# Optimization experiments

Hardware: AMD Instinct MI355X
Metric: run time of the kernel (lower is better)

## Reference

```python
import jax, jax.numpy as jnp
import numpy as np

M, N, D, B, LAYERS = 512, 512, 1024, 4096, 16


def setup_inputs() -> dict:
    key = jax.random.key(0)
    ks = jax.random.split(key, 4)
    x = jax.random.normal(ks[0], (M, B), dtype=jnp.float32)
    A = jax.random.normal(ks[1], (M, D), dtype=jnp.float32) / np.float32(np.sqrt(M))
    # fc[k].weight = A.t() + 0.001*randn  -> shape [d, m]
    W = A.T[None] + 0.001 * jax.random.normal(ks[2], (LAYERS, D, M), dtype=jnp.float32)
    Z0 = (1.0 / D) * jax.random.uniform(ks[3], (D, B), dtype=jnp.float32)
    E0 = jnp.zeros((M, B), dtype=jnp.float32)
    L0 = jnp.zeros((M, B), dtype=jnp.float32)
    ones = jnp.ones((LAYERS,), dtype=jnp.float32)
    return {
        'x': x, 'A': A, 'W': W, 'Z0': Z0, 'E0': E0, 'L0': L0,
        'beta1': ones, 'beta2': ones, 'beta3': ones, 'ss2': ones,
        'active_para': 0.2 * ones, 'active_para1': 0.8 * ones,
    }


def _soft(v, t):
    # self_active: relu(v - t) - relu(-v - t)  (soft threshold)
    return jax.nn.relu(v - t) - jax.nn.relu(-v - t)


def reference(x, A, W, Z0, E0, L0, beta1, beta2, beta3, ss2, active_para, active_para1):
    K = W.shape[0]
    # k = 0 (learned branch)
    T0 = A @ Z0 + E0 - x                      # [m, B]
    Var0 = L0 + beta1[0] * T0
    Z1 = _soft(Z0 - W[0] @ Var0, active_para[0])  # [d, B]

    def step(carry, params):
        Zp, Ep, Lp = carry
        b1, b2, b3, s2, ap, ap1, Wk = params
        AZ = A @ Zp                            # [m, B]
        VVar = Lp + b2 * (AZ + Ep - x)
        En = _soft(Ep - s2 * VVar, ap1)
        Tn = AZ + En - x
        Ln = Lp + b3 * Tn
        Varn = Ln + b1 * Tn
        Zn = _soft(Zp - Wk @ Varn, ap)
        return (Zn, En, Ln), (Zn, En, Ln)

    params = (beta1[1:], beta2[:K - 1], beta3[:K - 1], ss2[:K - 1],
              active_para[1:], active_para1[:K - 1], W[1:])
    _, (Zs, Es, Ls) = jax.lax.scan(step, (Z1, E0, L0), params)
    Z_all = jnp.concatenate([Z1[None], Zs], axis=0)   # [K, d, B]
    E_all = jnp.concatenate([E0[None], Es], axis=0)   # [K, m, B]
    L_all = jnp.concatenate([L0[None], Ls], axis=0)   # [K, m, B]
    return Z_all, E_all, L_all
```

## Files before the change

kernel.cpp:

```cpp
#include <hip/hip_runtime.h>
#include <cstddef>

#define MDIM 512
#define DDIM 1024
#define BDIM 4096
#define NLAYERS 16

constexpr int BK = 16;

__device__ __forceinline__ float softf(float v, float t) {
  return copysignf(fmaxf(fabsf(v) - t, 0.0f), v);
}

template <int MODE, int K>
__global__ __launch_bounds__(256) void gemm_bc(
    const float* __restrict__ P, const float* __restrict__ Bm,
    const float* __restrict__ xg, const float* __restrict__ Ep,
    const float* __restrict__ Lp, const float* __restrict__ Zp,
    const float* __restrict__ beta1, const float* __restrict__ beta2,
    const float* __restrict__ beta3, const float* __restrict__ ss2,
    const float* __restrict__ apar, const float* __restrict__ apar1, int k,
    float* __restrict__ O0, float* __restrict__ O1, float* __restrict__ O2) {
  __shared__ __align__(16) float As[2][BK][32];
  __shared__ __align__(16) float Bs[2][BK][128];

  const int tid = threadIdx.x;
  const int lane = tid & 63;
  const int w = __builtin_amdgcn_readfirstlane((int)(tid >> 6));
  const int m0 = blockIdx.x * 32, n0 = blockIdx.y * 128;
  const int r0 = m0 + w * 8;
  const int c0 = n0 + lane * 2;

  float acc[8][2];
#pragma unroll
  for (int r = 0; r < 8; ++r) {
    acc[r][0] = 0.0f;
    acc[r][1] = 0.0f;
  }

  const int ar = tid >> 3, akc = (tid & 7) * 2;
  const float* gA = P + (size_t)(m0 + ar) * K + akc;
  const int br = tid >> 4, bc = (tid & 15) * 8;
  const float* gB = Bm + (size_t)br * BDIM + n0 + bc;

  float2 rA;
  float4 rB0, rB1;
  auto gload = [&](int k0) {
    rA = *reinterpret_cast<const float2*>(gA + (size_t)k0);
    rB0 = *reinterpret_cast<const float4*>(gB + (size_t)k0 * BDIM);
    rB1 = *reinterpret_cast<const float4*>(gB + (size_t)k0 * BDIM + 4);
  };
  auto stagewr = [&](int bb) {
    As[bb][akc][ar] = rA.x;
    As[bb][akc + 1][ar] = rA.y;
    *reinterpret_cast<float4*>(&Bs[bb][br][bc]) = rB0;
    *reinterpret_cast<float4*>(&Bs[bb][br][bc + 4]) = rB1;
  };
  auto comp = [&](int bb) {
#pragma unroll
    for (int kk = 0; kk < BK; ++kk) {
      const float4 a0 = *reinterpret_cast<const float4*>(&As[bb][kk][w * 8]);
      const float4 a1 =
          *reinterpret_cast<const float4*>(&As[bb][kk][w * 8 + 4]);
      const float a[8] = {a0.x, a0.y, a0.z, a0.w, a1.x, a1.y, a1.z, a1.w};
      const float2 b2 = *reinterpret_cast<const float2*>(&Bs[bb][kk][lane * 2]);
#pragma unroll
      for (int r = 0; r < 8; ++r) {
        acc[r][0] = fmaf(a[r], b2.x, acc[r][0]);
        acc[r][1] = fmaf(a[r], b2.y, acc[r][1]);
      }
    }
  };

  constexpr int NS = K / BK;
  gload(0);
  stagewr(0);
  __syncthreads();
  int bb = 0;
#pragma unroll 1
  for (int t = 1; t < NS; ++t) {
    gload(t * BK);
    comp(bb);
    stagewr(bb ^ 1);
    __syncthreads();
    bb ^= 1;
  }
  comp(bb);

  const float b1v = (MODE == 2) ? 0.f : beta1[k];
  float b2v = 0.f, b3v = 0.f, s2v = 0.f, a1v = 0.f, ap = 0.f;
  if (MODE == 1) {
    b2v = beta2[k - 1];
    b3v = beta3[k - 1];
    s2v = ss2[k - 1];
    a1v = apar1[k - 1];
  }
  if (MODE == 2) ap = apar[k];

#pragma unroll
  for (int r = 0; r < 8; ++r) {
    const size_t off = (size_t)(r0 + r) * BDIM + c0;
    if (MODE == 2) {
      const float2 z2 = *reinterpret_cast<const float2*>(&Zp[off]);
      float2 o;
      o.x = softf(z2.x - acc[r][0], ap);
      o.y = softf(z2.y - acc[r][1], ap);
      *reinterpret_cast<float2*>(&O0[off]) = o;
    } else {
      const float2 e2 = *reinterpret_cast<const float2*>(&Ep[off]);
      const float2 l2 = *reinterpret_cast<const float2*>(&Lp[off]);
      const float2 x2 = *reinterpret_cast<const float2*>(&xg[off]);
      const float ev[2] = {e2.x, e2.y};
      const float lv[2] = {l2.x, l2.y};
      const float xv[2] = {x2.x, x2.y};
      float vo[2], eo[2], lo_[2];
#pragma unroll
      for (int j = 0; j < 2; ++j) {
        const float az = acc[r][j];
        if (MODE == 0) {
          const float t0 = az + ev[j] - xv[j];
          vo[j] = fmaf(b1v, t0, lv[j]);
          eo[j] = ev[j];
          lo_[j] = lv[j];
        } else {
          const float vv = fmaf(b2v, az + ev[j] - xv[j], lv[j]);
          const float en = softf(ev[j] - s2v * vv, a1v);
          const float tn_ = az + en - xv[j];
          const float ln = fmaf(b3v, tn_, lv[j]);
          eo[j] = en;
          lo_[j] = ln;
          vo[j] = fmaf(b1v, tn_, ln);
        }
      }
      float2 t2;
      t2.x = vo[0];
      t2.y = vo[1];
      *reinterpret_cast<float2*>(&O0[off]) = t2;
      t2.x = eo[0];
      t2.y = eo[1];
      *reinterpret_cast<float2*>(&O1[off]) = t2;
      t2.x = lo_[0];
      t2.y = lo_[1];
      *reinterpret_cast<float2*>(&O2[off]) = t2;
    }
  }
}

extern "C" void kernel_launch(void* const* d_in, const int* in_sizes, int n_in,
                              void* d_out, int out_size, void* d_ws,
                              size_t ws_size, hipStream_t stream) {
  (void)in_sizes;
  (void)n_in;
  (void)out_size;
  (void)ws_size;
  const float* x = (const float*)d_in[0];
  const float* A = (const float*)d_in[1];
  const float* W = (const float*)d_in[2];
  const float* Z0 = (const float*)d_in[3];
  const float* E0 = (const float*)d_in[4];
  const float* L0 = (const float*)d_in[5];
  const float* beta1 = (const float*)d_in[6];
  const float* beta2 = (const float*)d_in[7];
  const float* beta3 = (const float*)d_in[8];
  const float* ss2 = (const float*)d_in[9];
  const float* apar = (const float*)d_in[10];
  const float* apar1 = (const float*)d_in[11];

  constexpr size_t DB = (size_t)DDIM * BDIM;
  constexpr size_t MB = (size_t)MDIM * BDIM;
  float* Zall = (float*)d_out;
  float* Eall = Zall + (size_t)NLAYERS * DB;
  float* Lall = Eall + (size_t)NLAYERS * MB;
  float* Var = (float*)d_ws;

  const dim3 blk(256);
  const dim3 gA(MDIM / 32, BDIM / 128);
  const dim3 gB(DDIM / 32, BDIM / 128);

  gemm_bc<0, DDIM><<<gA, blk, 0, stream>>>(
      A, Z0, x, E0, L0, nullptr, beta1, beta2, beta3, ss2, apar, apar1, 0, Var,
      Eall, Lall);
  gemm_bc<2, MDIM><<<gB, blk, 0, stream>>>(
      W, Var, nullptr, nullptr, nullptr, Z0, beta1, beta2, beta3, ss2, apar,
      apar1, 0, Zall, nullptr, nullptr);
  for (int k = 1; k < NLAYERS; ++k) {
    const float* Zp = Zall + (size_t)(k - 1) * DB;
    gemm_bc<1, DDIM><<<gA, blk, 0, stream>>>(
        A, Zp, x, Eall + (size_t)(k - 1) * MB, Lall + (size_t)(k - 1) * MB,
        nullptr, beta1, beta2, beta3, ss2, apar, apar1, k, Var,
        Eall + (size_t)k * MB, Lall + (size_t)k * MB);
    gemm_bc<2, MDIM><<<gB, blk, 0, stream>>>(
        W + (size_t)k * DDIM * MDIM, Var, nullptr, nullptr, nullptr, Zp, beta1,
        beta2, beta3, ss2, apar, apar1, k, Zall + (size_t)k * DB, nullptr,
        nullptr);
  }
}
```

Baseline: 2.445 ms.

## Shrink GEMM tile rows, add XCD-aware block remapping and occupancy hints

Halves the M-tile from 32 to 16 rows, so each thread now computes a 4x2 output block instead of 8x2 and the grid doubles. Block ids are remapped round-robin across the 8 XCDs so neighbouring tiles share an L2. Launch bounds now request a minimum number of waves per SIMD, and the B shared tile is padded to 132 columns. The intent is more blocks and higher occupancy to hide latency, at the cost of less register reuse per loaded B element and more total global traffic for B.

```diff
diff --git a/kernel.cpp b/kernel.cpp
--- a/kernel.cpp
+++ b/kernel.cpp
@@ -12,8 +12,8 @@
   return copysignf(fmaxf(fabsf(v) - t, 0.0f), v);
 }
 
-template <int MODE, int K>
-__global__ __launch_bounds__(256) void gemm_bc(
+template <int MODE, int K, int LOG2GX, int MINW>
+__global__ __launch_bounds__(256, MINW) void gemm_ho(
     const float* __restrict__ P, const float* __restrict__ Bm,
     const float* __restrict__ xg, const float* __restrict__ Ep,
     const float* __restrict__ Lp, const float* __restrict__ Zp,
@@ -21,51 +21,56 @@
     const float* __restrict__ beta3, const float* __restrict__ ss2,
     const float* __restrict__ apar, const float* __restrict__ apar1, int k,
     float* __restrict__ O0, float* __restrict__ O1, float* __restrict__ O2) {
-  __shared__ __align__(16) float As[2][BK][32];
-  __shared__ __align__(16) float Bs[2][BK][128];
+  __shared__ __align__(16) float As[2][BK][16];
+  __shared__ __align__(16) float Bs[2][BK][132];
 
   const int tid = threadIdx.x;
   const int lane = tid & 63;
   const int w = __builtin_amdgcn_readfirstlane((int)(tid >> 6));
-  const int m0 = blockIdx.x * 32, n0 = blockIdx.y * 128;
-  const int r0 = m0 + w * 8;
+
+  const int nwg = gridDim.x * gridDim.y;
+  const int bid = blockIdx.x + gridDim.x * blockIdx.y;
+  const int cpx = nwg >> 3;
+  const int lgc = (bid & 7) * cpx + (bid >> 3);
+  const int bx = lgc & ((1 << LOG2GX) - 1);
+  const int by = lgc >> LOG2GX;
+
+  const int m0 = bx * 16, n0 = by * 128;
+  const int r0 = m0 + w * 4;
   const int c0 = n0 + lane * 2;
 
-  float acc[8][2];
-#pragma unroll
-  for (int r = 0; r < 8; ++r) {
+  float acc[4][2];
+#pragma unroll
+  for (int r = 0; r < 4; ++r) {
     acc[r][0] = 0.0f;
     acc[r][1] = 0.0f;
   }
 
-  const int ar = tid >> 3, akc = (tid & 7) * 2;
-  const float* gA = P + (size_t)(m0 + ar) * K + akc;
-  const int br = tid >> 4, bc = (tid & 15) * 8;
-  const float* gB = Bm + (size_t)br * BDIM + n0 + bc;
-
-  float2 rA;
+  const int arow = tid >> 4, ak = tid & 15;
+  const float* gA = P + (size_t)(m0 + arow) * K + ak;
+  const int brow = tid >> 4, bcol = (tid & 15) * 8;
+  const float* gB = Bm + (size_t)brow * BDIM + n0 + bcol;
+
+  float rA;
   float4 rB0, rB1;
   auto gload = [&](int k0) {
-    rA = *reinterpret_cast<const float2*>(gA + (size_t)k0);
+    rA = gA[(size_t)k0];
     rB0 = *reinterpret_cast<const float4*>(gB + (size_t)k0 * BDIM);
     rB1 = *reinterpret_cast<const float4*>(gB + (size_t)k0 * BDIM + 4);
   };
   auto stagewr = [&](int bb) {
-    As[bb][akc][ar] = rA.x;
-    As[bb][akc + 1][ar] = rA.y;
-    *reinterpret_cast<float4*>(&Bs[bb][br][bc]) = rB0;
-    *reinterpret_cast<float4*>(&Bs[bb][br][bc + 4]) = rB1;
+    As[bb][ak][arow] = rA;
+    *reinterpret_cast<float4*>(&Bs[bb][brow][bcol]) = rB0;
+    *reinterpret_cast<float4*>(&Bs[bb][brow][bcol + 4]) = rB1;
   };
   auto comp = [&](int bb) {
 #pragma unroll
     for (int kk = 0; kk < BK; ++kk) {
-      const float4 a0 = *reinterpret_cast<const float4*>(&As[bb][kk][w * 8]);
-      const float4 a1 =
-          *reinterpret_cast<const float4*>(&As[bb][kk][w * 8 + 4]);
-      const float a[8] = {a0.x, a0.y, a0.z, a0.w, a1.x, a1.y, a1.z, a1.w};
+      const float4 a4 = *reinterpret_cast<const float4*>(&As[bb][kk][w * 4]);
+      const float a[4] = {a4.x, a4.y, a4.z, a4.w};
       const float2 b2 = *reinterpret_cast<const float2*>(&Bs[bb][kk][lane * 2]);
 #pragma unroll
-      for (int r = 0; r < 8; ++r) {
+      for (int r = 0; r < 4; ++r) {
         acc[r][0] = fmaf(a[r], b2.x, acc[r][0]);
         acc[r][1] = fmaf(a[r], b2.y, acc[r][1]);
       }
@@ -98,7 +103,7 @@
   if (MODE == 2) ap = apar[k];
 
 #pragma unroll
-  for (int r = 0; r < 8; ++r) {
+  for (int r = 0; r < 4; ++r) {
     const size_t off = (size_t)(r0 + r) * BDIM + c0;
     if (MODE == 2) {
       const float2 z2 = *reinterpret_cast<const float2*>(&Zp[off]);
@@ -174,22 +179,22 @@
   float* Var = (float*)d_ws;
 
   const dim3 blk(256);
-  const dim3 gA(MDIM / 32, BDIM / 128);
-  const dim3 gB(DDIM / 32, BDIM / 128);
-
-  gemm_bc<0, DDIM><<<gA, blk, 0, stream>>>(
+  const dim3 gA(MDIM / 16, BDIM / 128);
+  const dim3 gB(DDIM / 16, BDIM / 128);
+
+  gemm_ho<0, DDIM, 5, 4><<<gA, blk, 0, stream>>>(
       A, Z0, x, E0, L0, nullptr, beta1, beta2, beta3, ss2, apar, apar1, 0, Var,
       Eall, Lall);
-  gemm_bc<2, MDIM><<<gB, blk, 0, stream>>>(
+  gemm_ho<2, MDIM, 6, 8><<<gB, blk, 0, stream>>>(
       W, Var, nullptr, nullptr, nullptr, Z0, beta1, beta2, beta3, ss2, apar,
       apar1, 0, Zall, nullptr, nullptr);
   for (int k = 1; k < NLAYERS; ++k) {
     const float* Zp = Zall + (size_t)(k - 1) * DB;
-    gemm_bc<1, DDIM><<<gA, blk, 0, stream>>>(
+    gemm_ho<1, DDIM, 5, 4><<<gA, blk, 0, stream>>>(
         A, Zp, x, Eall + (size_t)(k - 1) * MB, Lall + (size_t)(k - 1) * MB,
         nullptr, beta1, beta2, beta3, ss2, apar, apar1, k, Var,
         Eall + (size_t)k * MB, Lall + (size_t)k * MB);
-    gemm_bc<2, MDIM><<<gB, blk, 0, stream>>>(
+    gemm_ho<2, MDIM, 6, 8><<<gB, blk, 0, stream>>>(
         W + (size_t)k * DDIM * MDIM, Var, nullptr, nullptr, nullptr, Zp, beta1,
         beta2, beta3, ss2, apar, apar1, k, Zall + (size_t)k * DB, nullptr,
         nullptr);
```

Result: slower. 2.779 ms (+13.7%).

## Replace LDS-tiled GEMM with register-only packed-FMA GEMM using larger tiles

Applied to the files above, without the earlier changes.

Removes shared-memory staging and barriers from the GEMM. Each wave now loads its 16 rows of the left matrix directly from global memory; these addresses are wave-uniform, so the loads act as broadcasts. Each lane loads its own two columns of the right operand and accumulates with packed 2-wide FMAs (v_pk_fma_f32), with register double-buffering of k-chunks of two. The block tile grows to 64 rows and the launch grids shrink to match, trading LDS reuse and coalesced staging for many small global loads that lean on the cache, plus higher register pressure.

```diff
diff --git a/kernel.cpp b/kernel.cpp
--- a/kernel.cpp
+++ b/kernel.cpp
@@ -6,14 +6,14 @@
 #define BDIM 4096
 #define NLAYERS 16
 
-constexpr int BK = 16;
+typedef float f32x2 __attribute__((ext_vector_type(2)));
 
 __device__ __forceinline__ float softf(float v, float t) {
   return copysignf(fmaxf(fabsf(v) - t, 0.0f), v);
 }
 
 template <int MODE, int K>
-__global__ __launch_bounds__(256) void gemm_bc(
+__global__ __launch_bounds__(256, 2) void gemm_pk(
     const float* __restrict__ P, const float* __restrict__ Bm,
     const float* __restrict__ xg, const float* __restrict__ Ep,
     const float* __restrict__ Lp, const float* __restrict__ Zp,
@@ -21,71 +21,55 @@
     const float* __restrict__ beta3, const float* __restrict__ ss2,
     const float* __restrict__ apar, const float* __restrict__ apar1, int k,
     float* __restrict__ O0, float* __restrict__ O1, float* __restrict__ O2) {
-  __shared__ __align__(16) float As[2][BK][32];
-  __shared__ __align__(16) float Bs[2][BK][128];
-
   const int tid = threadIdx.x;
   const int lane = tid & 63;
   const int w = __builtin_amdgcn_readfirstlane((int)(tid >> 6));
-  const int m0 = blockIdx.x * 32, n0 = blockIdx.y * 128;
-  const int r0 = m0 + w * 8;
-  const int c0 = n0 + lane * 2;
+  const int m0 = blockIdx.x * 64 + w * 16;
+  const int c0 = blockIdx.y * 128 + lane * 2;
 
-  float acc[8][2];
+  const float* pA = P + (size_t)m0 * K;
+  const float* pB = Bm + c0;
+
+  f32x2 acc[16];
 #pragma unroll
-  for (int r = 0; r < 8; ++r) {
-    acc[r][0] = 0.0f;
-    acc[r][1] = 0.0f;
-  }
+  for (int r = 0; r < 16; ++r) acc[r] = (f32x2)(0.0f);
 
-  const int ar = tid >> 3, akc = (tid & 7) * 2;
-  const float* gA = P + (size_t)(m0 + ar) * K + akc;
-  const int br = tid >> 4, bc = (tid & 15) * 8;
-  const float* gB = Bm + (size_t)br * BDIM + n0 + bc;
+  f32x2 A0[16], A1[16], B0[2], B1[2];
 
-  float2 rA;
-  float4 rB0, rB1;
-  auto gload = [&](int k0) {
-    rA = *reinterpret_cast<const float2*>(gA + (size_t)k0);
-    rB0 = *reinterpret_cast<const float4*>(gB + (size_t)k0 * BDIM);
-    rB1 = *reinterpret_cast<const float4*>(gB + (size_t)k0 * BDIM + 4);
+  auto loadA = [&](f32x2(&Ab)[16], int k0) {
+#pragma unroll
+    for (int r = 0; r < 16; ++r)
+      Ab[r] = *reinterpret_cast<const f32x2*>(pA + (size_t)r * K + k0);
   };
-  auto stagewr = [&](int bb) {
-    As[bb][akc][ar] = rA.x;
-    As[bb][akc + 1][ar] = rA.y;
-    *reinterpret_cast<float4*>(&Bs[bb][br][bc]) = rB0;
-    *reinterpret_cast<float4*>(&Bs[bb][br][bc + 4]) = rB1;
+  auto loadB = [&](f32x2(&Bb)[2], int k0) {
+#pragma unroll
+    for (int j = 0; j < 2; ++j)
+      Bb[j] = *reinterpret_cast<const f32x2*>(pB + (size_t)(k0 + j) * BDIM);
   };
-  auto comp = [&](int bb) {
+  auto comp = [&](const f32x2(&Ab)[16], const f32x2(&Bb)[2]) {
 #pragma unroll
-    for (int kk = 0; kk < BK; ++kk) {
-      const float4 a0 = *reinterpret_cast<const float4*>(&As[bb][kk][w * 8]);
-      const float4 a1 =
-          *reinterpret_cast<const float4*>(&As[bb][kk][w * 8 + 4]);
-      const float a[8] = {a0.x, a0.y, a0.z, a0.w, a1.x, a1.y, a1.z, a1.w};
-      const float2 b2 = *reinterpret_cast<const float2*>(&Bs[bb][kk][lane * 2]);
+    for (int j = 0; j < 2; ++j)
 #pragma unroll
-      for (int r = 0; r < 8; ++r) {
-        acc[r][0] = fmaf(a[r], b2.x, acc[r][0]);
-        acc[r][1] = fmaf(a[r], b2.y, acc[r][1]);
+      for (int r = 0; r < 16; ++r) {
+        const f32x2 av = {Ab[r][j], Ab[r][j]};
+        acc[r] = __builtin_elementwise_fma(av, Bb[j], acc[r]);
       }
-    }
   };
 
-  constexpr int NS = K / BK;
-  gload(0);
-  stagewr(0);
-  __syncthreads();
-  int bb = 0;
+  constexpr int NCH = K / 2;
+  loadA(A0, 0);
+  loadB(B0, 0);
 #pragma unroll 1
-  for (int t = 1; t < NS; ++t) {
-    gload(t * BK);
-    comp(bb);
-    stagewr(bb ^ 1);
-    __syncthreads();
-    bb ^= 1;
+  for (int t = 0; t + 2 <= NCH; t += 2) {
+    loadA(A1, (t + 1) * 2);
+    loadB(B1, (t + 1) * 2);
+    comp(A0, B0);
+    if (t + 2 < NCH) {
+      loadA(A0, (t + 2) * 2);
+      loadB(B0, (t + 2) * 2);
+    }
+    comp(A1, B1);
   }
-  comp(bb);
 
   const float b1v = (MODE == 2) ? 0.f : beta1[k];
   float b2v = 0.f, b3v = 0.f, s2v = 0.f, a1v = 0.f, ap = 0.f;
@@ -98,8 +82,8 @@
   if (MODE == 2) ap = apar[k];
 
 #pragma unroll
-  for (int r = 0; r < 8; ++r) {
-    const size_t off = (size_t)(r0 + r) * BDIM + c0;
+  for (int r = 0; r < 16; ++r) {
+    const size_t off = (size_t)(m0 + r) * BDIM + c0;
     if (MODE == 2) {
       const float2 z2 = *reinterpret_cast<const float2*>(&Zp[off]);
       float2 o;
@@ -174,22 +158,22 @@
   float* Var = (float*)d_ws;
 
   const dim3 blk(256);
-  const dim3 gA(MDIM / 32, BDIM / 128);
-  const dim3 gB(DDIM / 32, BDIM / 128);
+  const dim3 gA(MDIM / 64, BDIM / 128);
+  const dim3 gB(DDIM / 64, BDIM / 128);
 
-  gemm_bc<0, DDIM><<<gA, blk, 0, stream>>>(
+  gemm_pk<0, DDIM><<<gA, blk, 0, stream>>>(
       A, Z0, x, E0, L0, nullptr, beta1, beta2, beta3, ss2, apar, apar1, 0, Var,
       Eall, Lall);
-  gemm_bc<2, MDIM><<<gB, blk, 0, stream>>>(
+  gemm_pk<2, MDIM><<<gB, blk, 0, stream>>>(
       W, Var, nullptr, nullptr, nullptr, Z0, beta1, beta2, beta3, ss2, apar,
       apar1, 0, Zall, nullptr, nullptr);
   for (int k = 1; k < NLAYERS; ++k) {
     const float* Zp = Zall + (size_t)(k - 1) * DB;
-    gemm_bc<1, DDIM><<<gA, blk, 0, stream>>>(
+    gemm_pk<1, DDIM><<<gA, blk, 0, stream>>>(
         A, Zp, x, Eall + (size_t)(k - 1) * MB, Lall + (size_t)(k - 1) * MB,
         nullptr, beta1, beta2, beta3, ss2, apar, apar1, k, Var,
         Eall + (size_t)k * MB, Lall + (size_t)k * MB);
-    gemm_bc<2, MDIM><<<gB, blk, 0, stream>>>(
+    gemm_pk<2, MDIM><<<gB, blk, 0, stream>>>(
         W + (size_t)k * DDIM * MDIM, Var, nullptr, nullptr, nullptr, Zp, beta1,
         beta2, beta3, ss2, apar, apar1, k, Zall + (size_t)k * DB, nullptr,
         nullptr);
```

Result: slower. 6.038 ms (+147.0%).

## Enlarge register tiles per thread in fused GEMM kernels

Applied to the files above, without the earlier changes.

Restructures the GEMM kernel so each thread computes an 8x(2*TNW) register tile instead of 8x2. The block M-tile grows to 64 rows for the A@Z GEMM and 128 rows for the W@Var GEMM. This raises the FMA-to-LDS-load ratio and cuts redundant global traffic on the B operand, which is re-read by fewer blocks. In exchange it uses more registers, which may lower occupancy, and the epilogue stores become strided scalar accesses split into two column groups.

```diff
diff --git a/kernel.cpp b/kernel.cpp
--- a/kernel.cpp
+++ b/kernel.cpp
@@ -12,8 +12,8 @@
   return copysignf(fmaxf(fabsf(v) - t, 0.0f), v);
 }
 
-template <int MODE, int K>
-__global__ __launch_bounds__(256) void gemm_bc(
+template <int MODE, int K, int TNW>
+__global__ __launch_bounds__(256) void gemm_rt(
     const float* __restrict__ P, const float* __restrict__ Bm,
     const float* __restrict__ xg, const float* __restrict__ Ep,
     const float* __restrict__ Lp, const float* __restrict__ Zp,
@@ -21,54 +21,77 @@
     const float* __restrict__ beta3, const float* __restrict__ ss2,
     const float* __restrict__ apar, const float* __restrict__ apar1, int k,
     float* __restrict__ O0, float* __restrict__ O1, float* __restrict__ O2) {
-  __shared__ __align__(16) float As[2][BK][32];
+  constexpr int BM = 32 * TNW;
+  constexpr int CT = 64 / TNW;
+  constexpr int APT = BM / 64;
+  __shared__ __align__(16) float As[2][BK][BM];
   __shared__ __align__(16) float Bs[2][BK][128];
 
   const int tid = threadIdx.x;
-  const int lane = tid & 63;
-  const int w = __builtin_amdgcn_readfirstlane((int)(tid >> 6));
-  const int m0 = blockIdx.x * 32, n0 = blockIdx.y * 128;
-  const int r0 = m0 + w * 8;
-  const int c0 = n0 + lane * 2;
-
-  float acc[8][2];
-#pragma unroll
-  for (int r = 0; r < 8; ++r) {
-    acc[r][0] = 0.0f;
-    acc[r][1] = 0.0f;
-  }
-
-  const int ar = tid >> 3, akc = (tid & 7) * 2;
+  const int tn = tid & (CT - 1);
+  const int tm = tid / CT;
+  const int m0 = blockIdx.x * BM, n0 = blockIdx.y * 128;
+
+  float acc[8][2][TNW];
+#pragma unroll
+  for (int r = 0; r < 8; ++r)
+#pragma unroll
+    for (int g = 0; g < 2; ++g)
+#pragma unroll
+      for (int j = 0; j < TNW; ++j) acc[r][g][j] = 0.0f;
+
+  const int ar = (APT == 1) ? (tid >> 2) : (tid >> 1);
+  const int akc = (APT == 1) ? ((tid & 3) * 4) : ((tid & 1) * 8);
   const float* gA = P + (size_t)(m0 + ar) * K + akc;
   const int br = tid >> 4, bc = (tid & 15) * 8;
   const float* gB = Bm + (size_t)br * BDIM + n0 + bc;
 
-  float2 rA;
-  float4 rB0, rB1;
+  float4 rA0, rA1, rB0, rB1;
   auto gload = [&](int k0) {
-    rA = *reinterpret_cast<const float2*>(gA + (size_t)k0);
+    rA0 = *reinterpret_cast<const float4*>(gA + (size_t)k0);
+    if (APT == 2) rA1 = *reinterpret_cast<const float4*>(gA + (size_t)k0 + 4);
     rB0 = *reinterpret_cast<const float4*>(gB + (size_t)k0 * BDIM);
     rB1 = *reinterpret_cast<const float4*>(gB + (size_t)k0 * BDIM + 4);
   };
   auto stagewr = [&](int bb) {
-    As[bb][akc][ar] = rA.x;
-    As[bb][akc + 1][ar] = rA.y;
+    As[bb][akc + 0][ar] = rA0.x;
+    As[bb][akc + 1][ar] = rA0.y;
+    As[bb][akc + 2][ar] = rA0.z;
+    As[bb][akc + 3][ar] = rA0.w;
+    if (APT == 2) {
+      As[bb][akc + 4][ar] = rA1.x;
+      As[bb][akc + 5][ar] = rA1.y;
+      As[bb][akc + 6][ar] = rA1.z;
+      As[bb][akc + 7][ar] = rA1.w;
+    }
     *reinterpret_cast<float4*>(&Bs[bb][br][bc]) = rB0;
     *reinterpret_cast<float4*>(&Bs[bb][br][bc + 4]) = rB1;
   };
   auto comp = [&](int bb) {
 #pragma unroll
     for (int kk = 0; kk < BK; ++kk) {
-      const float4 a0 = *reinterpret_cast<const float4*>(&As[bb][kk][w * 8]);
+      const float4 a0 = *reinterpret_cast<const float4*>(&As[bb][kk][tm * 8]);
       const float4 a1 =
-          *reinterpret_cast<const float4*>(&As[bb][kk][w * 8 + 4]);
+          *reinterpret_cast<const float4*>(&As[bb][kk][tm * 8 + 4]);
       const float a[8] = {a0.x, a0.y, a0.z, a0.w, a1.x, a1.y, a1.z, a1.w};
-      const float2 b2 = *reinterpret_cast<const float2*>(&Bs[bb][kk][lane * 2]);
-#pragma unroll
-      for (int r = 0; r < 8; ++r) {
-        acc[r][0] = fmaf(a[r], b2.x, acc[r][0]);
-        acc[r][1] = fmaf(a[r], b2.y, acc[r][1]);
+      float bv[2][TNW];
+#pragma unroll
+      for (int g = 0; g < 2; ++g) {
+        if (TNW == 4) {
+          *reinterpret_cast<float4*>(&bv[g][0]) =
+              *reinterpret_cast<const float4*>(&Bs[bb][kk][g * 64 + tn * 4]);
+        } else {
+          *reinterpret_cast<float2*>(&bv[g][0]) =
+              *reinterpret_cast<const float2*>(&Bs[bb][kk][g * 64 + tn * 2]);
+        }
       }
+#pragma unroll
+      for (int r = 0; r < 8; ++r)
+#pragma unroll
+        for (int g = 0; g < 2; ++g)
+#pragma unroll
+          for (int j = 0; j < TNW; ++j)
+            acc[r][g][j] = fmaf(a[r], bv[g][j], acc[r][g][j]);
     }
   };
 
@@ -99,49 +122,53 @@
 
 #pragma unroll
   for (int r = 0; r < 8; ++r) {
-    const size_t off = (size_t)(r0 + r) * BDIM + c0;
-    if (MODE == 2) {
-      const float2 z2 = *reinterpret_cast<const float2*>(&Zp[off]);
-      float2 o;
-      o.x = softf(z2.x - acc[r][0], ap);
-      o.y = softf(z2.y - acc[r][1], ap);
-      *reinterpret_cast<float2*>(&O0[off]) = o;
-    } else {
-      const float2 e2 = *reinterpret_cast<const float2*>(&Ep[off]);
-      const float2 l2 = *reinterpret_cast<const float2*>(&Lp[off]);
-      const float2 x2 = *reinterpret_cast<const float2*>(&xg[off]);
-      const float ev[2] = {e2.x, e2.y};
-      const float lv[2] = {l2.x, l2.y};
-      const float xv[2] = {x2.x, x2.y};
-      float vo[2], eo[2], lo_[2];
-#pragma unroll
-      for (int j = 0; j < 2; ++j) {
-        const float az = acc[r][j];
-        if (MODE == 0) {
-          const float t0 = az + ev[j] - xv[j];
-          vo[j] = fmaf(b1v, t0, lv[j]);
-          eo[j] = ev[j];
-          lo_[j] = lv[j];
-        } else {
-          const float vv = fmaf(b2v, az + ev[j] - xv[j], lv[j]);
-          const float en = softf(ev[j] - s2v * vv, a1v);
-          const float tn_ = az + en - xv[j];
-          const float ln = fmaf(b3v, tn_, lv[j]);
-          eo[j] = en;
-          lo_[j] = ln;
-          vo[j] = fmaf(b1v, tn_, ln);
+    const int row = m0 + tm * 8 + r;
+#pragma unroll
+    for (int g = 0; g < 2; ++g) {
+      const int col = n0 + g * 64 + tn * TNW;
+      const size_t off = (size_t)row * BDIM + col;
+      if (MODE == 2) {
+        float z[TNW], o[TNW];
+#pragma unroll
+        for (int j = 0; j < TNW; ++j) z[j] = Zp[off + j];
+#pragma unroll
+        for (int j = 0; j < TNW; ++j) o[j] = softf(z[j] - acc[r][g][j], ap);
+#pragma unroll
+        for (int j = 0; j < TNW; ++j) O0[off + j] = o[j];
+      } else {
+        float ev[TNW], lv[TNW], xv[TNW];
+#pragma unroll
+        for (int j = 0; j < TNW; ++j) {
+          ev[j] = Ep[off + j];
+          lv[j] = Lp[off + j];
+          xv[j] = xg[off + j];
+        }
+        float vo[TNW], eo[TNW], lo_[TNW];
+#pragma unroll
+        for (int j = 0; j < TNW; ++j) {
+          const float az = acc[r][g][j];
+          if (MODE == 0) {
+            const float t0 = az + ev[j] - xv[j];
+            vo[j] = fmaf(b1v, t0, lv[j]);
+            eo[j] = ev[j];
+            lo_[j] = lv[j];
+          } else {
+            const float vv = fmaf(b2v, az + ev[j] - xv[j], lv[j]);
+            const float en = softf(ev[j] - s2v * vv, a1v);
+            const float tn_ = az + en - xv[j];
+            const float ln = fmaf(b3v, tn_, lv[j]);
+            eo[j] = en;
+            lo_[j] = ln;
+            vo[j] = fmaf(b1v, tn_, ln);
+          }
+        }
+#pragma unroll
+        for (int j = 0; j < TNW; ++j) {
+          O0[off + j] = vo[j];
+          O1[off + j] = eo[j];
+          O2[off + j] = lo_[j];
         }
       }
-      float2 t2;
-      t2.x = vo[0];
-      t2.y = vo[1];
-      *reinterpret_cast<float2*>(&O0[off]) = t2;
-      t2.x = eo[0];
-      t2.y = eo[1];
-      *reinterpret_cast<float2*>(&O1[off]) = t2;
-      t2.x = lo_[0];
-      t2.y = lo_[1];
-      *reinterpret_cast<float2*>(&O2[off]) = t2;
     }
   }
 }
@@ -174,22 +201,22 @@
   float* Var = (float*)d_ws;
 
   const dim3 blk(256);
-  const dim3 gA(MDIM / 32, BDIM / 128);
-  const dim3 gB(DDIM / 32, BDIM / 128);
-
-  gemm_bc<0, DDIM><<<gA, blk, 0, stream>>>(
+  const dim3 gA(MDIM / 64, BDIM / 128);
+  const dim3 gB(DDIM / 128, BDIM / 128);
+
+  gemm_rt<0, DDIM, 2><<<gA, blk, 0, stream>>>(
       A, Z0, x, E0, L0, nullptr, beta1, beta2, beta3, ss2, apar, apar1, 0, Var,
       Eall, Lall);
-  gemm_bc<2, MDIM><<<gB, blk, 0, stream>>>(
+  gemm_rt<2, MDIM, 4><<<gB, blk, 0, stream>>>(
       W, Var, nullptr, nullptr, nullptr, Z0, beta1, beta2, beta3, ss2, apar,
       apar1, 0, Zall, nullptr, nullptr);
   for (int k = 1; k < NLAYERS; ++k) {
     const float* Zp = Zall + (size_t)(k - 1) * DB;
-    gemm_bc<1, DDIM><<<gA, blk, 0, stream>>>(
+    gemm_rt<1, DDIM, 2><<<gA, blk, 0, stream>>>(
         A, Zp, x, Eall + (size_t)(k - 1) * MB, Lall + (size_t)(k - 1) * MB,
         nullptr, beta1, beta2, beta3, ss2, apar, apar1, k, Var,
         Eall + (size_t)k * MB, Lall + (size_t)k * MB);
-    gemm_bc<2, MDIM><<<gB, blk, 0, stream>>>(
+    gemm_rt<2, MDIM, 4><<<gB, blk, 0, stream>>>(
         W + (size_t)k * DDIM * MDIM, Var, nullptr, nullptr, nullptr, Zp, beta1,
         beta2, beta3, ss2, apar, apar1, k, Zall + (size_t)k * DB, nullptr,
         nullptr);
```

Measured after the change: 2.282 ms. 1.07x faster.
